# Kernel tuning notes

Hardware: AMD Instinct MI355X
Metric: run time of the kernel (lower is better)

The kernel has to match this reference:

```python
import jax, jax.numpy as jnp
import numpy as np

N_CLUSTERS = 16
CLUSTER_SIZE = 32
N_HIDDEN = 16
N_FEATURES = N_CLUSTERS * CLUSTER_SIZE  # 512
BATCH = 131072


def setup_inputs() -> dict:
    key = jax.random.key(0)
    k_x, k_perm, k_ew, k_eb, k_dw, k_db = jax.random.split(key, 6)
    x = jax.random.normal(k_x, (BATCH, N_FEATURES), dtype=jnp.float32)
    # disjoint random feature clusters (a permutation split into groups)
    clusters = jax.random.permutation(k_perm, N_FEATURES).reshape(
        N_CLUSTERS, CLUSTER_SIZE).astype(jnp.int32)
    s_e = 1.0 / np.sqrt(CLUSTER_SIZE)
    s_d = 1.0 / np.sqrt(N_HIDDEN)
    enc_w = jax.random.uniform(k_ew, (N_CLUSTERS, N_HIDDEN, CLUSTER_SIZE),
                               minval=-s_e, maxval=s_e, dtype=jnp.float32)
    enc_b = jax.random.uniform(k_eb, (N_CLUSTERS, N_HIDDEN),
                               minval=-s_e, maxval=s_e, dtype=jnp.float32)
    dec_w = jax.random.uniform(k_dw, (N_CLUSTERS, CLUSTER_SIZE, N_HIDDEN),
                               minval=-s_d, maxval=s_d, dtype=jnp.float32)
    dec_b = jax.random.uniform(k_db, (N_CLUSTERS, CLUSTER_SIZE),
                               minval=-s_d, maxval=s_d, dtype=jnp.float32)
    return {"x": x, "clusters": clusters, "enc_w": enc_w, "enc_b": enc_b,
            "dec_w": dec_w, "dec_b": dec_b}


def reference(x, clusters, enc_w, enc_b, dec_w, dec_b):
    # gather per-cluster feature columns: [B, nC, cs]
    xi = x[:, clusters]
    # encoder: Linear(cs -> h) per cluster
    h = jnp.einsum('bnc,nhc->bnh', xi, enc_w) + enc_b  # [B, nC, h]
    # decoder: Linear(h -> cs) per cluster
    y = jnp.einsum('bnh,nch->bnc', h, dec_w) + dec_b   # [B, nC, cs]
    # concat cluster outputs along feature dim (cluster order)
    return y.reshape(x.shape[0], -1)  # [B, nC*cs]
```

## Files before the change

kernel.cpp:

```cpp
#include <hip/hip_runtime.h>


#define B_ROWS   131072
#define F        512
#define NC       16
#define CS       32
#define NH       16
#define NBLOCKS  1024
#define RPB      128
#define RPI      4
#define NITER    (RPB / RPI)

__global__ __launch_bounds__(256, 4)
void ensemble_kernel(const float* __restrict__ x,
                     const int*   __restrict__ clusters,
                     const float* __restrict__ enc_w,
                     const float* __restrict__ enc_b,
                     const float* __restrict__ dec_w,
                     const float* __restrict__ dec_b,
                     float*       __restrict__ out) {
    __shared__ float s_xi[2][RPI][F];
    __shared__ int   s_tgt[F];

    const int t = threadIdx.x;

    for (int j = t; j < F; j += 256) {
        int col = clusters[j];
        int nn = j >> 5, cc = j & 31;
        s_tgt[col] = (nn << 5) | ((cc + (nn << 2)) & 31);
    }
    __syncthreads();

    const int cbase = (t & 127) << 2;
    const int tgt0 = s_tgt[cbase + 0];
    const int tgt1 = s_tgt[cbase + 1];
    const int tgt2 = s_tgt[cbase + 2];
    const int tgt3 = s_tgt[cbase + 3];

    const int n  = t >> 4;
    const int c0 = (t & 15) << 1;
    const int rhalf = t >> 7;
    const int row_block = blockIdx.x * RPB;

    const float* xp = x + (size_t)(row_block + rhalf) * F + cbase;
    const int xioff = n << 5;
    float* op = out + (size_t)row_block * F + xioff + c0;

    float4 v[2];
    v[0] = *(const float4*)(xp);
    v[1] = *(const float4*)(xp + 2 * F);
    xp += RPI * F;

    float m0[32], m1[32];
    #pragma unroll
    for (int i = 0; i < 32; ++i) { m0[i] = 0.f; m1[i] = 0.f; }
    float b0 = dec_b[n * CS + c0];
    float b1 = dec_b[n * CS + c0 + 1];

    for (int h = 0; h < NH; ++h) {
        const float d0 = dec_w[(n * CS + c0)     * NH + h];
        const float d1 = dec_w[(n * CS + c0 + 1) * NH + h];
        const float eb = enc_b[n * NH + h];
        b0 += d0 * eb;
        b1 += d1 * eb;
        const float4* ew = (const float4*)(enc_w + (n * NH + h) * CS);
        #pragma unroll
        for (int k = 0; k < 8; ++k) {
            float4 e = ew[k];
            m0[4*k+0] += d0 * e.x;  m1[4*k+0] += d1 * e.x;
            m0[4*k+1] += d0 * e.y;  m1[4*k+1] += d1 * e.y;
            m0[4*k+2] += d0 * e.z;  m1[4*k+2] += d1 * e.z;
            m0[4*k+3] += d0 * e.w;  m1[4*k+3] += d1 * e.w;
        }
    }

    {
        float* d0p = s_xi[0][0 * 2 + rhalf];
        d0p[tgt0] = v[0].x; d0p[tgt1] = v[0].y; d0p[tgt2] = v[0].z; d0p[tgt3] = v[0].w;
        float* d1p = s_xi[0][1 * 2 + rhalf];
        d1p[tgt0] = v[1].x; d1p[tgt1] = v[1].y; d1p[tgt2] = v[1].z; d1p[tgt3] = v[1].w;
    }
    __syncthreads();

    for (int it = 0; it < NITER - 1; ++it) {
        const int cur = it & 1;

        v[0] = *(const float4*)(xp);
        v[1] = *(const float4*)(xp + 2 * F);
        xp += RPI * F;

        #pragma unroll
        for (int r = 0; r < RPI; ++r) {
            float a0 = b0, a1 = b1;
            const float* xr = &s_xi[cur][r][xioff];
            #pragma unroll
            for (int k = 0; k < 8; ++k) {
                const int kk = (k + n) & 7;
                float4 xv = *(const float4*)(xr + (kk << 2));
                a0 += m0[4*k+0] * xv.x;  a1 += m1[4*k+0] * xv.x;
                a0 += m0[4*k+1] * xv.y;  a1 += m1[4*k+1] * xv.y;
                a0 += m0[4*k+2] * xv.z;  a1 += m1[4*k+2] * xv.z;
                a0 += m0[4*k+3] * xv.w;  a1 += m1[4*k+3] * xv.w;
            }
            *(float2*)(op + r * F) = make_float2(a0, a1);
        }
        op += RPI * F;

        {
            float* d0p = s_xi[cur ^ 1][0 * 2 + rhalf];
            d0p[tgt0] = v[0].x; d0p[tgt1] = v[0].y; d0p[tgt2] = v[0].z; d0p[tgt3] = v[0].w;
            float* d1p = s_xi[cur ^ 1][1 * 2 + rhalf];
            d1p[tgt0] = v[1].x; d1p[tgt1] = v[1].y; d1p[tgt2] = v[1].z; d1p[tgt3] = v[1].w;
        }
        __syncthreads();
    }

    {
        const int cur = (NITER - 1) & 1;
        #pragma unroll
        for (int r = 0; r < RPI; ++r) {
            float a0 = b0, a1 = b1;
            const float* xr = &s_xi[cur][r][xioff];
            #pragma unroll
            for (int k = 0; k < 8; ++k) {
                const int kk = (k + n) & 7;
                float4 xv = *(const float4*)(xr + (kk << 2));
                a0 += m0[4*k+0] * xv.x;  a1 += m1[4*k+0] * xv.x;
                a0 += m0[4*k+1] * xv.y;  a1 += m1[4*k+1] * xv.y;
                a0 += m0[4*k+2] * xv.z;  a1 += m1[4*k+2] * xv.z;
                a0 += m0[4*k+3] * xv.w;  a1 += m1[4*k+3] * xv.w;
            }
            *(float2*)(op + r * F) = make_float2(a0, a1);
        }
    }
}

extern "C" void kernel_launch(void* const* d_in, const int* in_sizes, int n_in,
                              void* d_out, int out_size, void* d_ws, size_t ws_size,
                              hipStream_t stream) {
    const float* x      = (const float*)d_in[0];
    const int*   clus   = (const int*)  d_in[1];
    const float* enc_w  = (const float*)d_in[2];
    const float* enc_b  = (const float*)d_in[3];
    const float* dec_w  = (const float*)d_in[4];
    const float* dec_b  = (const float*)d_in[5];
    float*       out    = (float*)d_out;

    ensemble_kernel<<<NBLOCKS, 256, 0, stream>>>(x, clus, enc_w, enc_b, dec_w, dec_b, out);
}
```

Before: 470.8 us.

## Replace LDS row reads with DPP lane rotation across cluster lanes

Each thread now loads only its own two gathered inputs from shared memory and rotates them across the 16 lanes of its cluster using DPP row_ror. It no longer reads all 32 inputs of the cluster from LDS. The fused encoder-decoder weight matrix is precomputed in a rotation-indexed order that matches. This cuts LDS read traffic and instructions, at the cost of about 30 extra DPP moves per row. It also relies on the DPP rotation direction being detected correctly at runtime.

```diff
diff --git a/kernel.cpp b/kernel.cpp
--- a/kernel.cpp
+++ b/kernel.cpp
@@ -10,6 +10,11 @@
 #define RPB      128
 #define RPI      4
 #define NITER    (RPB / RPI)
+
+__device__ __forceinline__ float ror1_f(float v) {
+    return __int_as_float(__builtin_amdgcn_update_dpp(
+        0, __float_as_int(v), 0x121 , 0xF, 0xF, false));
+}
 
 __global__ __launch_bounds__(256, 4)
 void ensemble_kernel(const float* __restrict__ x,
@@ -24,11 +29,7 @@
 
     const int t = threadIdx.x;
 
-    for (int j = t; j < F; j += 256) {
-        int col = clusters[j];
-        int nn = j >> 5, cc = j & 31;
-        s_tgt[col] = (nn << 5) | ((cc + (nn << 2)) & 31);
-    }
+    for (int j = t; j < F; j += 256) s_tgt[clusters[j]] = j;
     __syncthreads();
 
     const int cbase = (t & 127) << 2;
@@ -38,40 +39,57 @@
     const int tgt3 = s_tgt[cbase + 3];
 
     const int n  = t >> 4;
-    const int c0 = (t & 15) << 1;
+    const int lc = t & 15;
     const int rhalf = t >> 7;
     const int row_block = blockIdx.x * RPB;
 
     const float* xp = x + (size_t)(row_block + rhalf) * F + cbase;
-    const int xioff = n << 5;
-    float* op = out + (size_t)row_block * F + xioff + c0;
+    const int xioff = (n << 5) + (lc << 1);
+    float* op = out + (size_t)row_block * F + xioff;
 
     float4 v[2];
     v[0] = *(const float4*)(xp);
     v[1] = *(const float4*)(xp + 2 * F);
     xp += RPI * F;
 
-    float m0[32], m1[32];
+    const int sl = __builtin_amdgcn_update_dpp(0, lc, 0x121, 0xF, 0xF, false);
+    const int d  = (((sl - lc) & 15) == 1) ? 1 : 15;
+
+    float dw0[NH], dw1[NH];
+    {
+        const float4* p0 = (const float4*)(dec_w + (size_t)(n * CS + (lc << 1))     * NH);
+        const float4* p1 = (const float4*)(dec_w + (size_t)(n * CS + (lc << 1) + 1) * NH);
+        #pragma unroll
+        for (int q = 0; q < 4; ++q) {
+            float4 a = p0[q];
+            dw0[4*q+0] = a.x; dw0[4*q+1] = a.y; dw0[4*q+2] = a.z; dw0[4*q+3] = a.w;
+            float4 b = p1[q];
+            dw1[4*q+0] = b.x; dw1[4*q+1] = b.y; dw1[4*q+2] = b.z; dw1[4*q+3] = b.w;
+        }
+    }
+
+    float b0 = dec_b[n * CS + (lc << 1)];
+    float b1 = dec_b[n * CS + (lc << 1) + 1];
     #pragma unroll
-    for (int i = 0; i < 32; ++i) { m0[i] = 0.f; m1[i] = 0.f; }
-    float b0 = dec_b[n * CS + c0];
-    float b1 = dec_b[n * CS + c0 + 1];
+    for (int h = 0; h < NH; ++h) {
+        const float eb = enc_b[n * NH + h];
+        b0 += dw0[h] * eb;
+        b1 += dw1[h] * eb;
+    }
 
-    for (int h = 0; h < NH; ++h) {
-        const float d0 = dec_w[(n * CS + c0)     * NH + h];
-        const float d1 = dec_w[(n * CS + c0 + 1) * NH + h];
-        const float eb = enc_b[n * NH + h];
-        b0 += d0 * eb;
-        b1 += d1 * eb;
-        const float4* ew = (const float4*)(enc_w + (n * NH + h) * CS);
+    float mA0[16], mA1[16], mB0[16], mB1[16];
+    #pragma unroll
+    for (int s = 0; s < 16; ++s) {
+        const int cp = ((lc + d * s) & 15) << 1;
+        const float* ep = enc_w + (size_t)n * NH * CS + cp;
+        float a0 = 0.f, a1 = 0.f, c0 = 0.f, c1 = 0.f;
         #pragma unroll
-        for (int k = 0; k < 8; ++k) {
-            float4 e = ew[k];
-            m0[4*k+0] += d0 * e.x;  m1[4*k+0] += d1 * e.x;
-            m0[4*k+1] += d0 * e.y;  m1[4*k+1] += d1 * e.y;
-            m0[4*k+2] += d0 * e.z;  m1[4*k+2] += d1 * e.z;
-            m0[4*k+3] += d0 * e.w;  m1[4*k+3] += d1 * e.w;
+        for (int h = 0; h < NH; ++h) {
+            const float2 ev = *(const float2*)(ep + h * CS);
+            a0 += dw0[h] * ev.x;  a1 += dw0[h] * ev.y;
+            c0 += dw1[h] * ev.x;  c1 += dw1[h] * ev.y;
         }
+        mA0[s] = a0; mA1[s] = a1; mB0[s] = c0; mB1[s] = c1;
     }
 
     {
@@ -91,16 +109,16 @@
 
         #pragma unroll
         for (int r = 0; r < RPI; ++r) {
+            const float2 xv = *(const float2*)(&s_xi[cur][r][xioff]);
+            float x0 = xv.x, x1 = xv.y;
             float a0 = b0, a1 = b1;
-            const float* xr = &s_xi[cur][r][xioff];
             #pragma unroll
-            for (int k = 0; k < 8; ++k) {
-                const int kk = (k + n) & 7;
-                float4 xv = *(const float4*)(xr + (kk << 2));
-                a0 += m0[4*k+0] * xv.x;  a1 += m1[4*k+0] * xv.x;
-                a0 += m0[4*k+1] * xv.y;  a1 += m1[4*k+1] * xv.y;
-                a0 += m0[4*k+2] * xv.z;  a1 += m1[4*k+2] * xv.z;
-                a0 += m0[4*k+3] * xv.w;  a1 += m1[4*k+3] * xv.w;
+            for (int s = 0; s < 16; ++s) {
+                a0 += mA0[s] * x0;
+                a1 += mB0[s] * x0;
+                a0 += mA1[s] * x1;
+                a1 += mB1[s] * x1;
+                if (s < 15) { x0 = ror1_f(x0); x1 = ror1_f(x1); }
             }
             *(float2*)(op + r * F) = make_float2(a0, a1);
         }
@@ -119,16 +137,16 @@
         const int cur = (NITER - 1) & 1;
         #pragma unroll
         for (int r = 0; r < RPI; ++r) {
+            const float2 xv = *(const float2*)(&s_xi[cur][r][xioff]);
+            float x0 = xv.x, x1 = xv.y;
             float a0 = b0, a1 = b1;
-            const float* xr = &s_xi[cur][r][xioff];
             #pragma unroll
-            for (int k = 0; k < 8; ++k) {
-                const int kk = (k + n) & 7;
-                float4 xv = *(const float4*)(xr + (kk << 2));
-                a0 += m0[4*k+0] * xv.x;  a1 += m1[4*k+0] * xv.x;
-                a0 += m0[4*k+1] * xv.y;  a1 += m1[4*k+1] * xv.y;
-                a0 += m0[4*k+2] * xv.z;  a1 += m1[4*k+2] * xv.z;
-                a0 += m0[4*k+3] * xv.w;  a1 += m1[4*k+3] * xv.w;
+            for (int s = 0; s < 16; ++s) {
+                a0 += mA0[s] * x0;
+                a1 += mB0[s] * x0;
+                a0 += mA1[s] * x1;
+                a1 += mB1[s] * x1;
+                if (s < 15) { x0 = ror1_f(x0); x1 = ror1_f(x1); }
             }
             *(float2*)(op + r * F) = make_float2(a0, a1);
         }
```

After: 520.2 us. 10.5% more time.
